# Kernel optimization log

Hardware: AMD Instinct MI355X
Metric: run time of the kernel (lower is better)

Reference implementation:

```python
import jax, jax.numpy as jnp
import numpy as np

N = 50000   # nodes
E = 640000  # edges
IN = 128
HID = 128
EPS = 1e-5


def setup_inputs() -> dict:
    key = jax.random.key(0)
    ks = jax.random.split(key, 8)
    s = 1.0 / np.sqrt(IN)
    inp = {
        "x": jax.random.normal(ks[0], (N, IN), jnp.float32),
        "src": jax.random.randint(ks[1], (E,), 0, N, dtype=jnp.int32),
        "dst": jax.random.randint(ks[2], (E,), 0, N, dtype=jnp.int32),
        "W1": jax.random.normal(ks[3], (IN, HID), jnp.float32) * s,
        "b1": jnp.zeros((HID,), jnp.float32),
        "g1": jnp.ones((HID,), jnp.float32),
        "be1": jnp.zeros((HID,), jnp.float32),
        "W2": jax.random.normal(ks[4], (HID, HID), jnp.float32) * s,
        "b2": jnp.zeros((HID,), jnp.float32),
        "g2": jnp.ones((HID,), jnp.float32),
        "be2": jnp.zeros((HID,), jnp.float32),
        "W3": jax.random.normal(ks[5], (HID, HID), jnp.float32) * s,
        "b3": jnp.zeros((HID,), jnp.float32),
        "g3": jnp.ones((HID,), jnp.float32),
        "be3": jnp.zeros((HID,), jnp.float32),
    }
    return inp


def _layernorm(h, g, b):
    mu = jnp.mean(h, axis=-1, keepdims=True)
    var = jnp.mean(jnp.square(h - mu), axis=-1, keepdims=True)
    return g * (h - mu) * jax.lax.rsqrt(var + EPS) + b


def _gcn_conv(h, W, b, src, dst):
    # Kipf & Welling GCN: D^{-1/2} (A + I) D^{-1/2} (H W) + b
    # self-loops added with weight 1; degree computed on the target index.
    hw = h @ W                                          # [N, HID]
    deg = jax.ops.segment_sum(jnp.ones((E,), h.dtype), dst, num_segments=N) + 1.0
    dinv = jax.lax.rsqrt(deg)                           # deg >= 1 due to self loop
    msg = hw[src] * (dinv[src] * dinv[dst])[:, None]    # gather + normalize, [E, HID]
    agg = jax.ops.segment_sum(msg, dst, num_segments=N)  # scatter-add
    agg = agg + hw * (dinv * dinv)[:, None]             # self-loop contribution
    return agg + b


def reference(x, src, dst, W1, b1, g1, be1, W2, b2, g2, be2, W3, b3, g3, be3):
    layers = [(W1, b1, g1, be1), (W2, b2, g2, be2), (W3, b3, g3, be3)]
    h = x
    for i, (W, b, g, be) in enumerate(layers):
        h_in = h
        h = _gcn_conv(h, W, b, src, dst)
        h = _layernorm(h, g, be)
        h = jax.nn.relu(h)
        # dropout: eval mode -> identity
        if i > 0 and h.shape == h_in.shape:
            h = h + h_in
    return h
```

## Files before the change

### kernel.cpp

```cpp
#include <hip/hip_runtime.h>
#include <hip/hip_bf16.h>

#define NFEAT 128
#define EPSLN 1e-5f
#define PAD 64

typedef __attribute__((ext_vector_type(8))) short short8;
typedef __attribute__((ext_vector_type(4))) float f32x4;

__device__ __forceinline__ float bf2f(ushort u) {
    union { uint u32; float f; } v; v.u32 = ((uint)u) << 16; return v.f;
}
__device__ __forceinline__ ushort f2bf(float f) {
    union { float f; uint u32; } v; v.f = f;
    uint u = v.u32;
    u += 0x7FFF + ((u >> 16) & 1);
    return (ushort)(u >> 16);
}

__global__ void setup_kernel(const float* __restrict__ x, ushort* __restrict__ xb, int n4,
                             int4* __restrict__ cnt4, int ncnt4,
                             const float* __restrict__ W0, const float* __restrict__ W1,
                             const float* __restrict__ W2,
                             ushort* __restrict__ Wt0, ushort* __restrict__ Wt1,
                             ushort* __restrict__ Wt2) {
    int i = blockIdx.x * 256 + threadIdx.x;
    if (i < n4) {
        float4 v = ((const float4*)x)[i];
        ushort4 o;
        o.x = f2bf(v.x); o.y = f2bf(v.y); o.z = f2bf(v.z); o.w = f2bf(v.w);
        ((ushort4*)xb)[i] = o;
    }
    if (i < ncnt4) cnt4[i] = make_int4(0, 0, 0, 0);
    if (i < 3 * NFEAT * NFEAT) {
        int l = i / (NFEAT * NFEAT);
        int r = i - l * (NFEAT * NFEAT);
        int k = r >> 7, n = r & 127;
        const float* W = (l == 0) ? W0 : (l == 1) ? W1 : W2;
        ushort* Wt = (l == 0) ? Wt0 : (l == 1) ? Wt1 : Wt2;
        Wt[n * NFEAT + k] = f2bf(W[r]);
    }
}

__global__ void fill_kernel(const int* __restrict__ src, const int* __restrict__ dst,
                            int* __restrict__ cnt, int* __restrict__ csr, int E) {
    int e = blockIdx.x * 256 + threadIdx.x;
    if (e < E) {
        int d = dst[e];
        int s = src[e];
        int pos = atomicAdd(&cnt[d], 1);
        if (pos < PAD) csr[d * PAD + pos] = s;
    }
}

__global__ __launch_bounds__(256) void gemm_mfma_kernel(const ushort* __restrict__ hb,
                                                        const ushort* __restrict__ Wt,
                                                        const int* __restrict__ cnt,
                                                        ushort* __restrict__ hw, int N) {
    __shared__ ushort WtL[NFEAT * NFEAT];
    {
        const uint4* src4 = (const uint4*)Wt;
        uint4* dst4 = (uint4*)WtL;
        #pragma unroll
        for (int i = 0; i < 8; ++i)
            dst4[threadIdx.x + i * 256] = src4[threadIdx.x + i * 256];
    }
    __syncthreads();

    const int wave = threadIdx.x >> 6;
    const int lane = threadIdx.x & 63;
    const int quad = lane >> 4;
    const int l16  = lane & 15;
    const int row0 = blockIdx.x * 128 + wave * 32;

    short8 afrag[2][4];
    #pragma unroll
    for (int t = 0; t < 2; ++t) {
        const int arow = row0 + t * 16 + l16;
        const short8* ap = (const short8*)(hb + (size_t)arow * NFEAT);
        const bool rowok = (arow < N);
        #pragma unroll
        for (int ks = 0; ks < 4; ++ks) {
            if (rowok) afrag[t][ks] = ap[ks * 4 + quad];
            else       afrag[t][ks] = short8{0, 0, 0, 0, 0, 0, 0, 0};
        }
    }

    f32x4 acc[2][8];
    #pragma unroll
    for (int t = 0; t < 2; ++t)
        #pragma unroll
        for (int ct = 0; ct < 8; ++ct) acc[t][ct] = f32x4{0.f, 0.f, 0.f, 0.f};

    #pragma unroll
    for (int ct = 0; ct < 8; ++ct) {
        const int bcol = ct * 16 + l16;
        const short8* bp = (const short8*)(WtL + (size_t)bcol * NFEAT);
        #pragma unroll
        for (int ks = 0; ks < 4; ++ks) {
            short8 bfrag = bp[ks * 4 + quad];
            acc[0][ct] = __builtin_amdgcn_mfma_f32_16x16x32_bf16(afrag[0][ks], bfrag, acc[0][ct], 0, 0, 0);
            acc[1][ct] = __builtin_amdgcn_mfma_f32_16x16x32_bf16(afrag[1][ks], bfrag, acc[1][ct], 0, 0, 0);
        }
    }

    #pragma unroll
    for (int t = 0; t < 2; ++t) {
        const int orow_base = row0 + t * 16 + quad * 4;
        #pragma unroll
        for (int r = 0; r < 4; ++r) {
            const int orow = orow_base + r;
            if (orow < N) {
                const float di = rsqrtf((float)cnt[orow] + 1.0f);
                ushort* op = hw + (size_t)orow * NFEAT + l16;
                #pragma unroll
                for (int ct = 0; ct < 8; ++ct)
                    op[ct * 16] = f2bf(acc[t][ct][r] * di);
            }
        }
    }
}

__global__ __launch_bounds__(256) void agg_ln_kernel(const ushort* __restrict__ hwb,
                                                     const int* __restrict__ cnt,
                                                     const int* __restrict__ csr,
                                                     const float* __restrict__ bias,
                                                     const float* __restrict__ gamma,
                                                     const float* __restrict__ beta,
                                                     const ushort* __restrict__ hres_b,
                                                     float* __restrict__ outf,
                                                     ushort* __restrict__ outb,
                                                     int N) {
    const int node = blockIdx.x * 4 + (threadIdx.x >> 6);
    const int lane = threadIdx.x & 63;
    if (node >= N) return;
    const int quad = lane >> 4;
    const int l16  = lane & 15;

    const int cn  = cnt[node];
    const int deg = (cn < PAD) ? cn : PAD;
    const float di = rsqrtf((float)cn + 1.0f);
    const int* ce = csr + (size_t)node * PAD;
    const uint4* hw4 = (const uint4*)hwb;

    float acc[8];
    #pragma unroll
    for (int i = 0; i < 8; ++i) acc[i] = 0.f;

    const int ng = (deg + 7) >> 3;
    for (int gi = 0; gi < ng; ++gi) {
        const int j0 = gi * 8 + quad;
        const int j1 = j0 + 4;
        int s0 = 0, s1 = 0;
        float w0 = 0.f, w1 = 0.f;
        if (j0 < deg) { s0 = ce[j0]; w0 = 1.f; }
        if (j1 < deg) { s1 = ce[j1]; w1 = 1.f; }
        uint4 v0 = hw4[(size_t)s0 * 16 + l16];
        uint4 v1 = hw4[(size_t)s1 * 16 + l16];
        acc[0] = fmaf(bf2f((ushort)(v0.x & 0xFFFF)), w0, acc[0]);
        acc[1] = fmaf(bf2f((ushort)(v0.x >> 16)),   w0, acc[1]);
        acc[2] = fmaf(bf2f((ushort)(v0.y & 0xFFFF)), w0, acc[2]);
        acc[3] = fmaf(bf2f((ushort)(v0.y >> 16)),   w0, acc[3]);
        acc[4] = fmaf(bf2f((ushort)(v0.z & 0xFFFF)), w0, acc[4]);
        acc[5] = fmaf(bf2f((ushort)(v0.z >> 16)),   w0, acc[5]);
        acc[6] = fmaf(bf2f((ushort)(v0.w & 0xFFFF)), w0, acc[6]);
        acc[7] = fmaf(bf2f((ushort)(v0.w >> 16)),   w0, acc[7]);
        acc[0] = fmaf(bf2f((ushort)(v1.x & 0xFFFF)), w1, acc[0]);
        acc[1] = fmaf(bf2f((ushort)(v1.x >> 16)),   w1, acc[1]);
        acc[2] = fmaf(bf2f((ushort)(v1.y & 0xFFFF)), w1, acc[2]);
        acc[3] = fmaf(bf2f((ushort)(v1.y >> 16)),   w1, acc[3]);
        acc[4] = fmaf(bf2f((ushort)(v1.z & 0xFFFF)), w1, acc[4]);
        acc[5] = fmaf(bf2f((ushort)(v1.z >> 16)),   w1, acc[5]);
        acc[6] = fmaf(bf2f((ushort)(v1.w & 0xFFFF)), w1, acc[6]);
        acc[7] = fmaf(bf2f((ushort)(v1.w >> 16)),   w1, acc[7]);
    }

    #pragma unroll
    for (int i = 0; i < 8; ++i) {
        acc[i] += __shfl_xor(acc[i], 16);
        acc[i] += __shfl_xor(acc[i], 32);
    }

    const int c0i = l16 * 8;
    uint4 hv = hw4[(size_t)node * 16 + l16];
    float4 b0 = ((const float4*)(bias + c0i))[0];
    float4 b1 = ((const float4*)(bias + c0i))[1];
    float x[8];
    x[0] = (acc[0] + bf2f((ushort)(hv.x & 0xFFFF))) * di + b0.x;
    x[1] = (acc[1] + bf2f((ushort)(hv.x >> 16)))   * di + b0.y;
    x[2] = (acc[2] + bf2f((ushort)(hv.y & 0xFFFF))) * di + b0.z;
    x[3] = (acc[3] + bf2f((ushort)(hv.y >> 16)))   * di + b0.w;
    x[4] = (acc[4] + bf2f((ushort)(hv.z & 0xFFFF))) * di + b1.x;
    x[5] = (acc[5] + bf2f((ushort)(hv.z >> 16)))   * di + b1.y;
    x[6] = (acc[6] + bf2f((ushort)(hv.w & 0xFFFF))) * di + b1.z;
    x[7] = (acc[7] + bf2f((ushort)(hv.w >> 16)))   * di + b1.w;

    float s = 0.f, sq = 0.f;
    #pragma unroll
    for (int i = 0; i < 8; ++i) { s += x[i]; sq += x[i] * x[i]; }
    #pragma unroll
    for (int o = 8; o > 0; o >>= 1) {
        s  += __shfl_xor(s, o);
        sq += __shfl_xor(sq, o);
    }
    const float mu  = s * (1.0f / NFEAT);
    const float var = sq * (1.0f / NFEAT) - mu * mu;
    const float rs  = rsqrtf(var + EPSLN);

    float4 g0 = ((const float4*)(gamma + c0i))[0];
    float4 g1 = ((const float4*)(gamma + c0i))[1];
    float4 e0 = ((const float4*)(beta + c0i))[0];
    float4 e1 = ((const float4*)(beta + c0i))[1];
    float gm[8] = {g0.x, g0.y, g0.z, g0.w, g1.x, g1.y, g1.z, g1.w};
    float bt[8] = {e0.x, e0.y, e0.z, e0.w, e1.x, e1.y, e1.z, e1.w};

    float y[8];
    #pragma unroll
    for (int i = 0; i < 8; ++i)
        y[i] = fmaxf(gm[i] * (x[i] - mu) * rs + bt[i], 0.0f);

    if (hres_b) {
        uint4 hr = ((const uint4*)hres_b)[(size_t)node * 16 + l16];
        y[0] += bf2f((ushort)(hr.x & 0xFFFF));
        y[1] += bf2f((ushort)(hr.x >> 16));
        y[2] += bf2f((ushort)(hr.y & 0xFFFF));
        y[3] += bf2f((ushort)(hr.y >> 16));
        y[4] += bf2f((ushort)(hr.z & 0xFFFF));
        y[5] += bf2f((ushort)(hr.z >> 16));
        y[6] += bf2f((ushort)(hr.w & 0xFFFF));
        y[7] += bf2f((ushort)(hr.w >> 16));
    }

    if (quad == 0) {
        if (outf) {
            float4* op = (float4*)(outf + (size_t)node * NFEAT + c0i);
            op[0] = make_float4(y[0], y[1], y[2], y[3]);
            op[1] = make_float4(y[4], y[5], y[6], y[7]);
        }
        if (outb) {
            uint4 ob;
            ob.x = (uint)f2bf(y[0]) | ((uint)f2bf(y[1]) << 16);
            ob.y = (uint)f2bf(y[2]) | ((uint)f2bf(y[3]) << 16);
            ob.z = (uint)f2bf(y[4]) | ((uint)f2bf(y[5]) << 16);
            ob.w = (uint)f2bf(y[6]) | ((uint)f2bf(y[7]) << 16);
            ((uint4*)outb)[(size_t)node * 16 + l16] = ob;
        }
    }
}

extern "C" void kernel_launch(void* const* d_in, const int* in_sizes, int n_in,
                              void* d_out, int out_size, void* d_ws, size_t ws_size,
                              hipStream_t stream) {
    const float* x   = (const float*)d_in[0];
    const int*   src = (const int*)d_in[1];
    const int*   dst = (const int*)d_in[2];
    const float* W[3]  = {(const float*)d_in[3], (const float*)d_in[7],  (const float*)d_in[11]};
    const float* b[3]  = {(const float*)d_in[4], (const float*)d_in[8],  (const float*)d_in[12]};
    const float* g[3]  = {(const float*)d_in[5], (const float*)d_in[9],  (const float*)d_in[13]};
    const float* be[3] = {(const float*)d_in[6], (const float*)d_in[10], (const float*)d_in[14]};

    const int N = in_sizes[0] / NFEAT;
    const int E = in_sizes[1];

    char* ws = (char*)d_ws;
    size_t off = 0;
    auto carve = [&](size_t bytes) -> char* {
        char* p = ws + off;
        off = (off + bytes + 255) & ~(size_t)255;
        return p;
    };
    const int ncnt4 = (N + 3) / 4;
    int*    cnt = (int*)   carve((size_t)ncnt4 * 4 * sizeof(int));
    int*    csr = (int*)   carve(((size_t)N * PAD + 64) * sizeof(int));
    ushort* hwb = (ushort*)carve((size_t)N * NFEAT * sizeof(ushort));
    ushort* xb  = (ushort*)carve((size_t)N * NFEAT * sizeof(ushort));
    ushort* h1b = (ushort*)carve((size_t)N * NFEAT * sizeof(ushort));
    ushort* h2b = (ushort*)carve((size_t)N * NFEAT * sizeof(ushort));
    ushort* Wt[3];
    for (int l = 0; l < 3; ++l) Wt[l] = (ushort*)carve(NFEAT * NFEAT * sizeof(ushort));
    (void)ws_size;

    const int n4 = N * NFEAT / 4;
    int setup_threads = n4;
    if (3 * NFEAT * NFEAT > setup_threads) setup_threads = 3 * NFEAT * NFEAT;
    if (ncnt4 > setup_threads) setup_threads = ncnt4;
    setup_kernel<<<(setup_threads + 255) / 256, 256, 0, stream>>>(
        x, xb, n4, (int4*)cnt, ncnt4, W[0], W[1], W[2], Wt[0], Wt[1], Wt[2]);

    fill_kernel<<<(E + 255) / 256, 256, 0, stream>>>(src, dst, cnt, csr, E);

    const ushort* hbin[3]  = {xb, h1b, h2b};
    const ushort* hresb[3] = {nullptr, h1b, h2b};
    float*        houtf[3] = {nullptr, nullptr, (float*)d_out};
    ushort*       houtb[3] = {h1b, h2b, nullptr};

    const int gemm_blocks = (N + 127) / 128;
    const int agg_blocks = (N + 3) / 4;

    for (int l = 0; l < 3; ++l) {
        gemm_mfma_kernel<<<gemm_blocks, 256, 0, stream>>>(hbin[l], Wt[l], cnt, hwb, N);
        agg_ln_kernel<<<agg_blocks, 256, 0, stream>>>(hwb, cnt, csr,
                                                      b[l], g[l], be[l],
                                                      hresb[l], houtf[l], houtb[l], N);
    }
}
```

Measured before the change: 282.7 us.

## Fuse fp32-to-bf16 input conversion into first GEMM and batch neighbor index loads

The separate pass that converted x to bf16 in the setup kernel is removed. The first-layer GEMM now reads fp32 rows directly and converts them in registers, which saves writing and rereading a bf16 copy of x. The aggregation kernel loads up to 64 CSR neighbor indices in one coalesced read per wave and distributes them with shuffles. It also processes 16 neighbors per iteration instead of 8, and the self feature load is hoisted ahead of the loop, all to expose more memory-level parallelism. The cost is extra register pressure and twice the A-operand read bytes in the layer-1 GEMM.

```diff
diff --git a/kernel.cpp b/kernel.cpp
--- a/kernel.cpp
+++ b/kernel.cpp
@@ -18,19 +18,12 @@
     return (ushort)(u >> 16);
 }
 
-__global__ void setup_kernel(const float* __restrict__ x, ushort* __restrict__ xb, int n4,
-                             int4* __restrict__ cnt4, int ncnt4,
+__global__ void setup_kernel(int4* __restrict__ cnt4, int ncnt4,
                              const float* __restrict__ W0, const float* __restrict__ W1,
                              const float* __restrict__ W2,
                              ushort* __restrict__ Wt0, ushort* __restrict__ Wt1,
                              ushort* __restrict__ Wt2) {
     int i = blockIdx.x * 256 + threadIdx.x;
-    if (i < n4) {
-        float4 v = ((const float4*)x)[i];
-        ushort4 o;
-        o.x = f2bf(v.x); o.y = f2bf(v.y); o.z = f2bf(v.z); o.w = f2bf(v.w);
-        ((ushort4*)xb)[i] = o;
-    }
     if (i < ncnt4) cnt4[i] = make_int4(0, 0, 0, 0);
     if (i < 3 * NFEAT * NFEAT) {
         int l = i / (NFEAT * NFEAT);
@@ -54,6 +47,7 @@
 }
 
 __global__ __launch_bounds__(256) void gemm_mfma_kernel(const ushort* __restrict__ hb,
+                                                        const float* __restrict__ hf,
                                                         const ushort* __restrict__ Wt,
                                                         const int* __restrict__ cnt,
                                                         ushort* __restrict__ hw, int N) {
@@ -77,12 +71,29 @@
     #pragma unroll
     for (int t = 0; t < 2; ++t) {
         const int arow = row0 + t * 16 + l16;
-        const short8* ap = (const short8*)(hb + (size_t)arow * NFEAT);
         const bool rowok = (arow < N);
-        #pragma unroll
-        for (int ks = 0; ks < 4; ++ks) {
-            if (rowok) afrag[t][ks] = ap[ks * 4 + quad];
-            else       afrag[t][ks] = short8{0, 0, 0, 0, 0, 0, 0, 0};
+        if (hf) {
+            const float4* fp = (const float4*)(hf + (size_t)arow * NFEAT);
+            #pragma unroll
+            for (int ks = 0; ks < 4; ++ks) {
+                short8 a = short8{0, 0, 0, 0, 0, 0, 0, 0};
+                if (rowok) {
+                    float4 u0 = fp[ks * 8 + quad * 2];
+                    float4 u1 = fp[ks * 8 + quad * 2 + 1];
+                    a[0] = (short)f2bf(u0.x); a[1] = (short)f2bf(u0.y);
+                    a[2] = (short)f2bf(u0.z); a[3] = (short)f2bf(u0.w);
+                    a[4] = (short)f2bf(u1.x); a[5] = (short)f2bf(u1.y);
+                    a[6] = (short)f2bf(u1.z); a[7] = (short)f2bf(u1.w);
+                }
+                afrag[t][ks] = a;
+            }
+        } else {
+            const short8* ap = (const short8*)(hb + (size_t)arow * NFEAT);
+            #pragma unroll
+            for (int ks = 0; ks < 4; ++ks) {
+                if (rowok) afrag[t][ks] = ap[ks * 4 + quad];
+                else       afrag[t][ks] = short8{0, 0, 0, 0, 0, 0, 0, 0};
+            }
         }
     }
 
@@ -136,6 +147,7 @@
     if (node >= N) return;
     const int quad = lane >> 4;
     const int l16  = lane & 15;
+    const int c0i  = l16 * 8;
 
     const int cn  = cnt[node];
     const int deg = (cn < PAD) ? cn : PAD;
@@ -143,20 +155,30 @@
     const int* ce = csr + (size_t)node * PAD;
     const uint4* hw4 = (const uint4*)hwb;
 
+    int myidx = 0;
+    if (lane < deg) myidx = ce[lane];
+
+    uint4 hv = hw4[(size_t)node * 16 + l16];
+
     float acc[8];
     #pragma unroll
     for (int i = 0; i < 8; ++i) acc[i] = 0.f;
 
-    const int ng = (deg + 7) >> 3;
+    const int ng = (deg + 15) >> 4;
     for (int gi = 0; gi < ng; ++gi) {
-        const int j0 = gi * 8 + quad;
-        const int j1 = j0 + 4;
-        int s0 = 0, s1 = 0;
-        float w0 = 0.f, w1 = 0.f;
-        if (j0 < deg) { s0 = ce[j0]; w0 = 1.f; }
-        if (j1 < deg) { s1 = ce[j1]; w1 = 1.f; }
+        const int jb = gi * 16 + quad;
+        const int s0 = __shfl(myidx, jb);
+        const int s1 = __shfl(myidx, jb + 4);
+        const int s2 = __shfl(myidx, jb + 8);
+        const int s3 = __shfl(myidx, jb + 12);
+        const float w0 = (jb      < deg) ? 1.f : 0.f;
+        const float w1 = (jb + 4  < deg) ? 1.f : 0.f;
+        const float w2 = (jb + 8  < deg) ? 1.f : 0.f;
+        const float w3 = (jb + 12 < deg) ? 1.f : 0.f;
         uint4 v0 = hw4[(size_t)s0 * 16 + l16];
         uint4 v1 = hw4[(size_t)s1 * 16 + l16];
+        uint4 v2 = hw4[(size_t)s2 * 16 + l16];
+        uint4 v3 = hw4[(size_t)s3 * 16 + l16];
         acc[0] = fmaf(bf2f((ushort)(v0.x & 0xFFFF)), w0, acc[0]);
         acc[1] = fmaf(bf2f((ushort)(v0.x >> 16)),   w0, acc[1]);
         acc[2] = fmaf(bf2f((ushort)(v0.y & 0xFFFF)), w0, acc[2]);
@@ -173,6 +195,22 @@
         acc[5] = fmaf(bf2f((ushort)(v1.z >> 16)),   w1, acc[5]);
         acc[6] = fmaf(bf2f((ushort)(v1.w & 0xFFFF)), w1, acc[6]);
         acc[7] = fmaf(bf2f((ushort)(v1.w >> 16)),   w1, acc[7]);
+        acc[0] = fmaf(bf2f((ushort)(v2.x & 0xFFFF)), w2, acc[0]);
+        acc[1] = fmaf(bf2f((ushort)(v2.x >> 16)),   w2, acc[1]);
+        acc[2] = fmaf(bf2f((ushort)(v2.y & 0xFFFF)), w2, acc[2]);
+        acc[3] = fmaf(bf2f((ushort)(v2.y >> 16)),   w2, acc[3]);
+        acc[4] = fmaf(bf2f((ushort)(v2.z & 0xFFFF)), w2, acc[4]);
+        acc[5] = fmaf(bf2f((ushort)(v2.z >> 16)),   w2, acc[5]);
+        acc[6] = fmaf(bf2f((ushort)(v2.w & 0xFFFF)), w2, acc[6]);
+        acc[7] = fmaf(bf2f((ushort)(v2.w >> 16)),   w2, acc[7]);
+        acc[0] = fmaf(bf2f((ushort)(v3.x & 0xFFFF)), w3, acc[0]);
+        acc[1] = fmaf(bf2f((ushort)(v3.x >> 16)),   w3, acc[1]);
+        acc[2] = fmaf(bf2f((ushort)(v3.y & 0xFFFF)), w3, acc[2]);
+        acc[3] = fmaf(bf2f((ushort)(v3.y >> 16)),   w3, acc[3]);
+        acc[4] = fmaf(bf2f((ushort)(v3.z & 0xFFFF)), w3, acc[4]);
+        acc[5] = fmaf(bf2f((ushort)(v3.z >> 16)),   w3, acc[5]);
+        acc[6] = fmaf(bf2f((ushort)(v3.w & 0xFFFF)), w3, acc[6]);
+        acc[7] = fmaf(bf2f((ushort)(v3.w >> 16)),   w3, acc[7]);
     }
 
     #pragma unroll
@@ -181,8 +219,6 @@
         acc[i] += __shfl_xor(acc[i], 32);
     }
 
-    const int c0i = l16 * 8;
-    uint4 hv = hw4[(size_t)node * 16 + l16];
     float4 b0 = ((const float4*)(bias + c0i))[0];
     float4 b1 = ((const float4*)(bias + c0i))[1];
     float x[8];
@@ -273,23 +309,21 @@
     int*    cnt = (int*)   carve((size_t)ncnt4 * 4 * sizeof(int));
     int*    csr = (int*)   carve(((size_t)N * PAD + 64) * sizeof(int));
     ushort* hwb = (ushort*)carve((size_t)N * NFEAT * sizeof(ushort));
-    ushort* xb  = (ushort*)carve((size_t)N * NFEAT * sizeof(ushort));
     ushort* h1b = (ushort*)carve((size_t)N * NFEAT * sizeof(ushort));
     ushort* h2b = (ushort*)carve((size_t)N * NFEAT * sizeof(ushort));
     ushort* Wt[3];
     for (int l = 0; l < 3; ++l) Wt[l] = (ushort*)carve(NFEAT * NFEAT * sizeof(ushort));
     (void)ws_size;
 
-    const int n4 = N * NFEAT / 4;
-    int setup_threads = n4;
-    if (3 * NFEAT * NFEAT > setup_threads) setup_threads = 3 * NFEAT * NFEAT;
+    int setup_threads = 3 * NFEAT * NFEAT;
     if (ncnt4 > setup_threads) setup_threads = ncnt4;
     setup_kernel<<<(setup_threads + 255) / 256, 256, 0, stream>>>(
-        x, xb, n4, (int4*)cnt, ncnt4, W[0], W[1], W[2], Wt[0], Wt[1], Wt[2]);
+        (int4*)cnt, ncnt4, W[0], W[1], W[2], Wt[0], Wt[1], Wt[2]);
 
     fill_kernel<<<(E + 255) / 256, 256, 0, stream>>>(src, dst, cnt, csr, E);
 
-    const ushort* hbin[3]  = {xb, h1b, h2b};
+    const ushort* hbin[3]  = {nullptr, h1b, h2b};
+    const float*  hfin[3]  = {x, nullptr, nullptr};
     const ushort* hresb[3] = {nullptr, h1b, h2b};
     float*        houtf[3] = {nullptr, nullptr, (float*)d_out};
     ushort*       houtb[3] = {h1b, h2b, nullptr};
@@ -298,7 +332,7 @@
     const int agg_blocks = (N + 3) / 4;
 
     for (int l = 0; l < 3; ++l) {
-        gemm_mfma_kernel<<<gemm_blocks, 256, 0, stream>>>(hbin[l], Wt[l], cnt, hwb, N);
+        gemm_mfma_kernel<<<gemm_blocks, 256, 0, stream>>>(hbin[l], hfin[l], Wt[l], cnt, hwb, N);
         agg_ln_kernel<<<agg_blocks, 256, 0, stream>>>(hwb, cnt, csr,
                                                       b[l], g[l], be[l],
                                                       hresb[l], houtf[l], houtb[l], N);
```

Result: faster. 270.3 us (-4.4%).
